# Performance work log

Measured on AMD Instinct MI355X. Metric: run time of the kernel, lower is better.

Reference implementation:

```python
import jax, jax.numpy as jnp
import numpy as np

B, S = 1, 2048
HIDDEN = 2560
NH, NKV, HD = 32, 8, 128
GS = 128  # awq group size
ROPE_THETA = 1000000.0


def dequant_q4(qweight, scales, qzeros):
    """Unpack int4 AWQ weights -> dense [K, N] float weight.
    qweight: [K//8, N] int32, 8 nibbles packed along the input (K) dim.
    scales/qzeros: [K//GS, N]. w = (nibble - zero) * scale.
    """
    K8, N = qweight.shape
    shifts = jnp.arange(8, dtype=jnp.int32) * 4
    nib = (qweight[:, None, :] >> shifts[None, :, None]) & 0xF  # [K//8, 8, N]
    w = nib.reshape(K8 * 8, N).astype(scales.dtype)             # [K, N]
    z = jnp.repeat(qzeros.astype(scales.dtype), GS, axis=0)     # [K, N]
    s = jnp.repeat(scales, GS, axis=0)                          # [K, N]
    return (w - z) * s


def linear_q4(x, qw, sc, qz, bias=None):
    w = dequant_q4(qw, sc, qz)                     # [K, N]
    y = jnp.einsum('bsk,kn->bsn', x, w)
    return y + bias if bias is not None else y


def rotate_half(x):
    x1, x2 = jnp.split(x, 2, axis=-1)
    return jnp.concatenate([-x2, x1], axis=-1)


def apply_rope(q, k, cos, sin):
    # cos/sin: [B, S, HD] -> broadcast over heads at dim 2
    c = cos[:, :, None, :]
    s = sin[:, :, None, :]
    return q * c + rotate_half(q) * s, k * c + rotate_half(k) * s


def setup_inputs() -> dict:
    key = jax.random.key(0)
    ks = jax.random.split(key, 12)

    x = jax.random.normal(ks[0], (B, S, HIDDEN), dtype=jnp.float32)

    # genuine rotary embedding tables
    inv_freq = 1.0 / (ROPE_THETA ** (np.arange(0, HD, 2, dtype=np.float32) / HD))
    t = np.arange(S, dtype=np.float32)
    freqs = np.outer(t, inv_freq)                      # [S, HD/2]
    emb = np.concatenate([freqs, freqs], axis=-1)      # [S, HD]
    cos = jnp.asarray(np.cos(emb)[None], dtype=jnp.float32)  # [1, S, HD]
    sin = jnp.asarray(np.sin(emb)[None], dtype=jnp.float32)

    def mk_proj(kq, ksc, kz, K, N, group=GS):
        qw = jax.random.randint(kq, (K // 8, N), 0, 2**31 - 1, dtype=jnp.int32)
        sc = jax.random.normal(ksc, (K // group, N), dtype=jnp.float32) * 0.01
        qz = jax.random.randint(kz, (K // group, N), 0, 16, dtype=jnp.int32)
        return qw, sc, qz

    q_qweight, q_scales, q_qzeros = mk_proj(ks[1], ks[2], ks[3], HIDDEN, NH * HD)
    k_qweight, k_scales, k_qzeros = mk_proj(ks[4], ks[5], ks[6], HIDDEN, NKV * HD)
    v_qweight, v_scales, v_qzeros = mk_proj(ks[7], ks[8], ks[9], HIDDEN, NKV * HD)
    o_qweight, o_scales, o_qzeros = mk_proj(ks[10], ks[11], jax.random.fold_in(key, 99), NH * HD, HIDDEN)

    kb = jax.random.split(jax.random.fold_in(key, 7), 3)
    q_bias = jax.random.normal(kb[0], (NH * HD,), dtype=jnp.float32) * 0.02
    k_bias = jax.random.normal(kb[1], (NKV * HD,), dtype=jnp.float32) * 0.02
    v_bias = jax.random.normal(kb[2], (NKV * HD,), dtype=jnp.float32) * 0.02

    return dict(x=x, cos=cos, sin=sin,
                q_scales=q_scales, q_bias=q_bias,
                k_scales=k_scales, k_bias=k_bias,
                v_scales=v_scales, v_bias=v_bias,
                o_scales=o_scales,
                q_qweight=q_qweight, q_qzeros=q_qzeros,
                k_qweight=k_qweight, k_qzeros=k_qzeros,
                v_qweight=v_qweight, v_qzeros=v_qzeros,
                o_qweight=o_qweight, o_qzeros=o_qzeros)


def reference(x, cos, sin,
              q_scales, q_bias, k_scales, k_bias, v_scales, v_bias, o_scales,
              q_qweight, q_qzeros, k_qweight, k_qzeros,
              v_qweight, v_qzeros, o_qweight, o_qzeros):
    b, s, _ = x.shape
    xq = linear_q4(x, q_qweight, q_scales, q_qzeros, q_bias).reshape(b, s, NH, HD)
    xk = linear_q4(x, k_qweight, k_scales, k_qzeros, k_bias).reshape(b, s, NKV, HD)
    xv = linear_q4(x, v_qweight, v_scales, v_qzeros, v_bias).reshape(b, s, NKV, HD)

    xq, xk = apply_rope(xq, xk, cos, sin)

    # GQA: repeat KV heads to match query heads (prefill, start_pos=0)
    rep = NH // NKV
    xk = jnp.repeat(xk, rep, axis=2)   # [b, s, NH, HD]
    xv = jnp.repeat(xv, rep, axis=2)

    scale = 1.0 / jnp.sqrt(jnp.asarray(HD, dtype=xq.dtype))
    scores = jnp.einsum('bqhd,bkhd->bhqk', xq, xk) * scale  # [b, NH, s, s]
    causal = jnp.tril(jnp.ones((s, s), dtype=bool))
    scores = jnp.where(causal[None, None], scores, jnp.finfo(scores.dtype).min)
    attn = jax.nn.softmax(scores, axis=-1)
    out = jnp.einsum('bhqk,bkhd->bqhd', attn, xv).reshape(b, s, NH * HD)

    return linear_q4(out, o_qweight, o_scales, o_qzeros)  # [b, s, HIDDEN]
```

## Files before the change

### kernel.cpp

```cpp
#include <hip/hip_runtime.h>
#include <hip/hip_bf16.h>
#include <cstdint>

#define S_LEN 2048
#define HIDDEN 2560
#define NH 32
#define NKV 8
#define HD 128
#define GS 128

typedef __attribute__((ext_vector_type(8))) _Float16 half8v;
typedef __attribute__((ext_vector_type(2))) _Float16 half2v;
typedef __attribute__((ext_vector_type(4))) float f32x4;
typedef unsigned int uint;
typedef unsigned short ushort;

__device__ inline ushort f2h(float f) {
    _Float16 h = (_Float16)f;
    return __builtin_bit_cast(ushort, h);
}
__device__ inline float h2f(ushort u) {
    return (float)__builtin_bit_cast(_Float16, u);
}
__device__ inline uint pk2(ushort a, ushort b) { return (uint)a | ((uint)b << 16); }

__device__ __attribute__((always_inline)) inline void gl_lds16(const void* g, void* l) {
    __builtin_amdgcn_global_load_lds(
        (const __attribute__((address_space(1))) unsigned int*)g,
        (__attribute__((address_space(3))) unsigned int*)l, 16, 0, 0);
}

#define WAIT_LGKM0  asm volatile("s_waitcnt lgkmcnt(0)" ::: "memory")
#define WAIT_VM(N)  asm volatile("s_waitcnt vmcnt(" #N ")" ::: "memory")
#define RAW_BARRIER { __builtin_amdgcn_s_barrier(); __builtin_amdgcn_sched_barrier(0); }

__global__ __launch_bounds__(256) void prep_kernel(
    const float* __restrict__ X, ushort* __restrict__ Xf,
    const int* __restrict__ q_qw, const float* __restrict__ q_sc, const int* __restrict__ q_qz,
    const int* __restrict__ k_qw, const float* __restrict__ k_sc, const int* __restrict__ k_qz,
    const int* __restrict__ v_qw, const float* __restrict__ v_sc, const int* __restrict__ v_qz,
    ushort* __restrict__ WT)
{
    __shared__ __align__(16) char Ts[16384];
    const int bid = blockIdx.x;
    const int t   = threadIdx.x;

    if (bid < 2560) {
        const size_t base = (size_t)bid * 2048 + (size_t)t * 8;
        float4 a = *(const float4*)&X[base];
        float4 b = *(const float4*)&X[base + 4];
        uint4 hw = {pk2(f2h(a.x), f2h(a.y)), pk2(f2h(a.z), f2h(a.w)),
                    pk2(f2h(b.x), f2h(b.y)), pk2(f2h(b.z), f2h(b.w))};
        *(uint4*)&Xf[base] = hw;
        return;
    }

    const int b2 = bid - 2560;
    const int bx = b2 % 96;
    const int kt = b2 / 96;

    int nloc0, wtbase, Nw;
    const int* QW; const float* SC; const int* QZ;
    if (bx < 64)      { Nw = NH * HD;  nloc0 = bx * 64;        wtbase = bx * 64;
                        QW = q_qw; SC = q_sc; QZ = q_qz; }
    else if (bx < 80) { Nw = NKV * HD; nloc0 = (bx - 64) * 64; wtbase = 4096 + nloc0;
                        QW = k_qw; SC = k_sc; QZ = k_qz; }
    else              { Nw = NKV * HD; nloc0 = (bx - 80) * 64; wtbase = 5120 + nloc0;
                        QW = v_qw; SC = v_sc; QZ = v_qz; }

    const int k80 = kt * 16;
    const int nn  = t & 63;
    const float scf = SC[(size_t)kt * Nw + nloc0 + nn];
    const float zf  = (float)QZ[(size_t)kt * Nw + nloc0 + nn];
    ushort sch = f2h(scf);
    float schf = h2f(sch);
    ushort msc = f2h(-128.0f * schf);
    ushort nzs = f2h(-(zf * schf));
    half2v S2 = {__builtin_bit_cast(_Float16, sch), __builtin_bit_cast(_Float16, sch)};
    half2v M2 = {__builtin_bit_cast(_Float16, msc), __builtin_bit_cast(_Float16, msc)};
    half2v Z2 = {__builtin_bit_cast(_Float16, nzs), __builtin_bit_cast(_Float16, nzs)};

#pragma unroll
    for (int i = 0; i < 4; ++i) {
        int kw = i * 4 + (t >> 6);
        uint q = (uint)QW[(size_t)(k80 + kw) * Nw + nloc0 + nn];
        uint xn = q & 0x0F0F0F0Fu;
        uint yn = (q >> 4) & 0x0F0F0F0Fu;
        uint W0 = __builtin_amdgcn_perm(yn, xn, 0x0C040C00u);
        uint W1 = __builtin_amdgcn_perm(yn, xn, 0x0C050C01u);
        uint W2 = __builtin_amdgcn_perm(yn, xn, 0x0C060C02u);
        uint W3 = __builtin_amdgcn_perm(yn, xn, 0x0C070C03u);
        uint e0 = (W0 << 3) | 0x58005800u;
        uint e1 = (W1 << 3) | 0x58005800u;
        uint e2 = (W2 << 3) | 0x58005800u;
        uint e3 = (W3 << 3) | 0x58005800u;
        half2v w0 = __builtin_bit_cast(half2v, e0) * S2 + M2; w0 = w0 + Z2;
        half2v w1 = __builtin_bit_cast(half2v, e1) * S2 + M2; w1 = w1 + Z2;
        half2v w2 = __builtin_bit_cast(half2v, e2) * S2 + M2; w2 = w2 + Z2;
        half2v w3 = __builtin_bit_cast(half2v, e3) * S2 + M2; w3 = w3 + Z2;
        uint4 dw = {__builtin_bit_cast(uint, w0), __builtin_bit_cast(uint, w1),
                    __builtin_bit_cast(uint, w2), __builtin_bit_cast(uint, w3)};
        *(uint4*)(Ts + nn * 256 + ((kw * 16) ^ ((nn & 7) << 4))) = dw;
    }
    __syncthreads();
    const int kc = t & 15;
#pragma unroll
    for (int i = 0; i < 4; ++i) {
        int nr = i * 16 + (t >> 4);
        uint4 v = *(const uint4*)(Ts + nr * 256 + ((kc * 16) ^ ((nr & 7) << 4)));
        *(uint4*)&WT[(size_t)(wtbase + nr) * HIDDEN + kt * 128 + kc * 8] = v;
    }
}

__global__ __launch_bounds__(256) void qkv12_kernel(
    const ushort* __restrict__ Xf, const ushort* __restrict__ WT,
    const float* __restrict__ q_b, const float* __restrict__ k_b,
    const float* __restrict__ v_b,
    const float* __restrict__ cosb, const float* __restrict__ sinb,
    ushort* __restrict__ Qf, ushort* __restrict__ Kf,
    ushort* __restrict__ VfT)
{
    __shared__ __align__(16) char LDSB[65536];
    ushort* A0 = (ushort*)(LDSB);
    ushort* A1 = (ushort*)(LDSB + 16384);
    ushort* B0 = (ushort*)(LDSB + 32768);
    ushort* B1 = (ushort*)(LDSB + 49152);

    const int t  = threadIdx.x;
    const int w  = t >> 6;
    const int l  = t & 63;
    const int lg = l >> 4;
    const int lr = l & 15;
    const int wr = w >> 1;
    const int wc = w & 1;
    const int K  = HIDDEN;

    const int bid  = blockIdx.x;
    const int xcd  = bid & 7;
    const int j    = bid >> 3;
    const int nblk = xcd * 6 + (j >> 4);
    const int m0   = (j & 15) * 128;
    const int wtrow = nblk * 128;

    int region, nbase;
    const float* BI;
    if (nblk < 32)      { region = 0; nbase = nblk * 128;        BI = q_b; }
    else if (nblk < 40) { region = 1; nbase = (nblk - 32) * 128; BI = k_b; }
    else                { region = 2; nbase = (nblk - 40) * 128; BI = v_b; }

    const int ldsAw = w * 1024;
    size_t aoff[4], boff[4];
#pragma unroll
    for (int i = 0; i < 4; ++i) {
        int slot = i * 256 + t;
        int rm = slot >> 3, rc = slot & 7;
        aoff[i] = (size_t)(m0 + rm) * K + (size_t)((rc ^ (rm & 7)) * 8);
        boff[i] = (size_t)(wtrow + rm) * K + (size_t)((rc ^ (rm & 7)) * 8);
    }

    int ncm[4];
#pragma unroll
    for (int nf = 0; nf < 4; ++nf)
        ncm[nf] = wc * 32 + (nf & 1) * 16 + lr + ((nf & 2) ? 64 : 0);

    const int xorA = (lr & 7) << 4;
    int aroff[4][2], broff[4][2];
#pragma unroll
    for (int mf = 0; mf < 4; ++mf)
#pragma unroll
        for (int ks = 0; ks < 2; ++ks)
            aroff[mf][ks] = (((wr * 64 + mf * 16 + lr) * 128) + lg * 16 + ks * 64) ^ xorA;
#pragma unroll
    for (int nf = 0; nf < 4; ++nf)
#pragma unroll
        for (int ks = 0; ks < 2; ++ks)
            broff[nf][ks] = ((ncm[nf] * 128) + lg * 16 + ks * 64) ^ xorA;

    f32x4 macc[4][4];
#pragma unroll
    for (int mf = 0; mf < 4; ++mf)
#pragma unroll
        for (int nf = 0; nf < 4; ++nf) macc[mf][nf] = f32x4{0.f, 0.f, 0.f, 0.f};

#define QKV_STAGE(AH, BH, k0) { \
    gl_lds16(Xf + (k0) + aoff[0], (char*)(AH) + ldsAw); \
    gl_lds16(Xf + (k0) + aoff[1], (char*)(AH) + 4096 + ldsAw); \
    gl_lds16(Xf + (k0) + aoff[2], (char*)(AH) + 8192 + ldsAw); \
    gl_lds16(Xf + (k0) + aoff[3], (char*)(AH) + 12288 + ldsAw); \
    gl_lds16(WT + (k0) + boff[0], (char*)(BH) + ldsAw); \
    gl_lds16(WT + (k0) + boff[1], (char*)(BH) + 4096 + ldsAw); \
    gl_lds16(WT + (k0) + boff[2], (char*)(BH) + 8192 + ldsAw); \
    gl_lds16(WT + (k0) + boff[3], (char*)(BH) + 12288 + ldsAw); }

#define QKV_COMPUTE(AH, BT) { \
    _Pragma("unroll") \
    for (int ks = 0; ks < 2; ++ks) { \
        half8v av[4], bv[4]; \
        _Pragma("unroll") \
        for (int mf = 0; mf < 4; ++mf) \
            av[mf] = *(const half8v*)((const char*)(AH) + aroff[mf][ks]); \
        _Pragma("unroll") \
        for (int nf = 0; nf < 4; ++nf) \
            bv[nf] = *(const half8v*)((const char*)(BT) + broff[nf][ks]); \
        _Pragma("unroll") \
        for (int mf = 0; mf < 4; ++mf) \
            _Pragma("unroll") \
            for (int nf = 0; nf < 4; ++nf) \
                macc[mf][nf] = __builtin_amdgcn_mfma_f32_16x16x32_f16(av[mf], bv[nf], macc[mf][nf], 0, 0, 0); \
    } }

    QKV_STAGE(A0, B0, 0);
    WAIT_VM(0);
    RAW_BARRIER;

    for (int g = 0; g < 19; ++g) {
        QKV_STAGE(A1, B1, (2 * g + 1) * 64);
        QKV_COMPUTE(A0, B0);
        WAIT_VM(0);
        RAW_BARRIER;
        QKV_STAGE(A0, B0, (2 * g + 2) * 64);
        QKV_COMPUTE(A1, B1);
        WAIT_VM(0);
        RAW_BARRIER;
    }
    QKV_STAGE(A1, B1, 39 * 64);
    QKV_COMPUTE(A0, B0);
    WAIT_VM(0);
    RAW_BARRIER;
    QKV_COMPUTE(A1, B1);

#pragma unroll
    for (int nf = 0; nf < 4; ++nf) {
        float bv = BI[nbase + ncm[nf]];
#pragma unroll
        for (int mf = 0; mf < 4; ++mf)
#pragma unroll
            for (int r = 0; r < 4; ++r) macc[mf][nf][r] += bv;
    }

    if (region == 2) {
        WAIT_LGKM0;
        RAW_BARRIER;
        ushort* EP = (ushort*)LDSB;
#pragma unroll
        for (int mf = 0; mf < 4; ++mf)
#pragma unroll
            for (int r = 0; r < 4; ++r) {
                int row = wr * 64 + mf * 16 + lg * 4 + r;
#pragma unroll
                for (int nf = 0; nf < 4; ++nf)
                    EP[row * 130 + ncm[nf]] = f2h(macc[mf][nf][r]);
            }
        WAIT_LGKM0;
        RAW_BARRIER;
        const int c   = t >> 1;
        const int seg = (t & 1) * 64;
        ushort* dst = &VfT[(size_t)(nbase + c) * S_LEN + m0 + seg];
#pragma unroll
        for (int g8 = 0; g8 < 8; ++g8) {
            ushort buf[8];
#pragma unroll
            for (int jj = 0; jj < 8; ++jj)
                buf[jj] = EP[(seg + g8 * 8 + jj) * 130 + c];
            *(uint4*)(dst + g8 * 8) = *(uint4*)buf;
        }
    } else {
        ushort* OF = (region == 0) ? Qf : Kf;
        const int No = (region == 0) ? NH * HD : NKV * HD;
        const float osc = (region == 0)
            ? 0.08838834764831845f * 1.44269504088896341f : 1.0f;
#pragma unroll
        for (int mf = 0; mf < 4; ++mf)
#pragma unroll
            for (int r = 0; r < 4; ++r) {
                int row = m0 + wr * 64 + mf * 16 + lg * 4 + r;
                const float* cb = &cosb[(size_t)row * HD];
                const float* sb = &sinb[(size_t)row * HD];
#pragma unroll
                for (int nf = 0; nf < 2; ++nf) {
                    int d = wc * 32 + nf * 16 + lr;
                    float a = macc[mf][nf][r];
                    float b = macc[mf][nf + 2][r];
                    float o1 = (a * cb[d]      - b * sb[d])      * osc;
                    float o2 = (b * cb[d + 64] + a * sb[d + 64]) * osc;
                    OF[(size_t)row * No + nbase + d]      = f2h(o1);
                    OF[(size_t)row * No + nbase + d + 64] = f2h(o2);
                }
            }
    }
#undef QKV_STAGE
#undef QKV_COMPUTE
}

__global__ __launch_bounds__(256) void oproj8_kernel(
    const ushort* __restrict__ Xb, const int* __restrict__ QW,
    const float* __restrict__ SC, const int* __restrict__ QZ,
    float* __restrict__ Y)
{
    __shared__ __align__(16) char LDSB[65536];
    ushort* A0 = (ushort*)(LDSB);
    ushort* A1 = (ushort*)(LDSB + 16384);
    ushort* B0 = (ushort*)(LDSB + 32768);
    ushort* B1 = (ushort*)(LDSB + 49152);

    const int t  = threadIdx.x;
    const int w  = t >> 6;
    const int l  = t & 63;
    const int lg = l >> 4;
    const int lr = l & 15;
    const int wr = w >> 1;
    const int wc = w & 1;
    const int K  = NH * HD;
    const int N  = HIDDEN;

    const int bid = blockIdx.x;
    const int swz = (bid & 7) * 40 + (bid >> 3);
    const int n0  = (swz % 20) * 128;
    const int m0  = (swz / 20) * 128;

    const int ldsAw = w * 1024;
    size_t aoff[4];
#pragma unroll
    for (int i = 0; i < 4; ++i) {
        int slot = i * 256 + t;
        int am = slot >> 3, ac = slot & 7;
        aoff[i] = (size_t)(m0 + am) * K + (size_t)((ac ^ (am & 7)) * 8);
    }
    const int bn  = t & 127;
    const int bk0 = (t >> 7) * 4;
    int bwoff[4];
#pragma unroll
    for (int j = 0; j < 4; ++j)
        bwoff[j] = (bn * 128 + (bk0 + j) * 16) ^ ((bn & 7) << 4);

    const int xorA = (lr & 7) << 4;
    int aroff[4][2], broff[4][2];
#pragma unroll
    for (int mf = 0; mf < 4; ++mf)
#pragma unroll
        for (int ks = 0; ks < 2; ++ks)
            aroff[mf][ks] = (((wr * 64 + mf * 16 + lr) * 128) + lg * 16 + ks * 64) ^ xorA;
#pragma unroll
    for (int nf = 0; nf < 4; ++nf)
#pragma unroll
        for (int ks = 0; ks < 2; ++ks)
            broff[nf][ks] = (((wc * 64 + nf * 16 + lr) * 128) + lg * 16 + ks * 64) ^ xorA;

    f32x4 macc[4][4];
#pragma unroll
    for (int mf = 0; mf < 4; ++mf)
#pragma unroll
        for (int nf = 0; nf < 4; ++nf) macc[mf][nf] = f32x4{0.f, 0.f, 0.f, 0.f};
    uint qr[4];
    float scf, zf;

#define OP_QW(tile) { int g8 = (tile) * 8; int gg = (tile) >> 1; \
    _Pragma("unroll") \
    for (int j = 0; j < 4; ++j) \
        qr[j] = (uint)QW[(size_t)(g8 + bk0 + j) * N + n0 + bn]; \
    scf = SC[(size_t)gg * N + n0 + bn]; \
    zf  = (float)QZ[(size_t)gg * N + n0 + bn]; }

#define OP_STAGE_A(AH, k0) { \
    gl_lds16(Xb + (k0) + aoff[0], (char*)(AH) + ldsAw); \
    gl_lds16(Xb + (k0) + aoff[1], (char*)(AH) + 4096 + ldsAw); \
    gl_lds16(Xb + (k0) + aoff[2], (char*)(AH) + 8192 + ldsAw); \
    gl_lds16(Xb + (k0) + aoff[3], (char*)(AH) + 12288 + ldsAw); }

#define OP_BWRITE(BT) { \
    ushort sch = f2h(scf); \
    float schf = h2f(sch); \
    ushort msc = f2h(-128.0f * schf); \
    ushort nzs = f2h(-(zf * schf)); \
    half2v S2 = {__builtin_bit_cast(_Float16, sch), __builtin_bit_cast(_Float16, sch)}; \
    half2v M2 = {__builtin_bit_cast(_Float16, msc), __builtin_bit_cast(_Float16, msc)}; \
    half2v Z2 = {__builtin_bit_cast(_Float16, nzs), __builtin_bit_cast(_Float16, nzs)}; \
    _Pragma("unroll") \
    for (int j = 0; j < 4; ++j) { \
        uint q = qr[j]; \
        uint xn = q & 0x0F0F0F0Fu; \
        uint yn = (q >> 4) & 0x0F0F0F0Fu; \
        uint4 dw; \
        uint W0 = __builtin_amdgcn_perm(yn, xn, 0x0C040C00u); \
        uint W1 = __builtin_amdgcn_perm(yn, xn, 0x0C050C01u); \
        uint W2 = __builtin_amdgcn_perm(yn, xn, 0x0C060C02u); \
        uint W3 = __builtin_amdgcn_perm(yn, xn, 0x0C070C03u); \
        uint e0 = (W0 << 3) | 0x58005800u; \
        uint e1 = (W1 << 3) | 0x58005800u; \
        uint e2 = (W2 << 3) | 0x58005800u; \
        uint e3 = (W3 << 3) | 0x58005800u; \
        half2v w0 = __builtin_bit_cast(half2v, e0) * S2 + M2; w0 = w0 + Z2; \
        half2v w1 = __builtin_bit_cast(half2v, e1) * S2 + M2; w1 = w1 + Z2; \
        half2v w2 = __builtin_bit_cast(half2v, e2) * S2 + M2; w2 = w2 + Z2; \
        half2v w3 = __builtin_bit_cast(half2v, e3) * S2 + M2; w3 = w3 + Z2; \
        dw.x = __builtin_bit_cast(uint, w0); \
        dw.y = __builtin_bit_cast(uint, w1); \
        dw.z = __builtin_bit_cast(uint, w2); \
        dw.w = __builtin_bit_cast(uint, w3); \
        *(uint4*)((char*)(BT) + bwoff[j]) = dw; \
    } }

#define OP_COMPUTE(AH, BT) { \
    _Pragma("unroll") \
    for (int ks = 0; ks < 2; ++ks) { \
        half8v av[4], bv[4]; \
        _Pragma("unroll") \
        for (int mf = 0; mf < 4; ++mf) \
            av[mf] = *(const half8v*)((const char*)(AH) + aroff[mf][ks]); \
        _Pragma("unroll") \
        for (int nf = 0; nf < 4; ++nf) \
            bv[nf] = *(const half8v*)((const char*)(BT) + broff[nf][ks]); \
        _Pragma("unroll") \
        for (int mf = 0; mf < 4; ++mf) \
            _Pragma("unroll") \
            for (int nf = 0; nf < 4; ++nf) \
                macc[mf][nf] = __builtin_amdgcn_mfma_f32_16x16x32_f16(av[mf], bv[nf], macc[mf][nf], 0, 0, 0); \
    } }

    OP_QW(0);
    OP_BWRITE(B0);
    OP_STAGE_A(A0, 0);
    OP_QW(1);
    WAIT_LGKM0;
    WAIT_VM(6);
    RAW_BARRIER;

    for (int g = 0; g < 31; ++g) {
        OP_STAGE_A(A1, (2 * g + 1) * 64);
        OP_COMPUTE(A0, B0);
        OP_BWRITE(B1);
        OP_QW(2 * g + 2);
        WAIT_LGKM0;
        WAIT_VM(6);
        RAW_BARRIER;
        OP_STAGE_A(A0, (2 * g + 2) * 64);
        OP_COMPUTE(A1, B1);
        OP_BWRITE(B0);
        OP_QW(2 * g + 3);
        WAIT_LGKM0;
        WAIT_VM(6);
        RAW_BARRIER;
    }
    OP_STAGE_A(A1, 63 * 64);
    OP_COMPUTE(A0, B0);
    OP_BWRITE(B1);
    WAIT_LGKM0;
    WAIT_VM(0);
    RAW_BARRIER;
    OP_COMPUTE(A1, B1);

#pragma unroll
    for (int mf = 0; mf < 4; ++mf)
#pragma unroll
        for (int r = 0; r < 4; ++r) {
            int row = m0 + wr * 64 + mf * 16 + lg * 4 + r;
#pragma unroll
            for (int nf = 0; nf < 4; ++nf)
                Y[(size_t)row * N + n0 + wc * 64 + nf * 16 + lr] = macc[mf][nf][r];
        }
#undef OP_QW
#undef OP_STAGE_A
#undef OP_BWRITE
#undef OP_COMPUTE
}

__global__ __launch_bounds__(256) void attn_mfma_kernel(
    const ushort* __restrict__ Qh,
    const ushort* __restrict__ Kh,
    const ushort* __restrict__ Vt,
    ushort* __restrict__ AO)
{
    __shared__ ushort Ks0[32 * 128];
    __shared__ ushort Ks1[32 * 128];
    __shared__ ushort Vs0[128 * 32];
    __shared__ ushort Vs1[128 * 32];
    __shared__ __align__(16) char PsB[4 * 1280];

    const int h  = blockIdx.x;
    const int qb = gridDim.y - 1 - blockIdx.y;
    const int s0 = qb * 64;
    const int t  = threadIdx.x;
    const int w  = t >> 6;
    const int l  = t & 63;
    const int lg = l >> 4;
    const int lr = l & 15;
    const int kvh = h >> 2;
    const int qw = s0 + w * 16;
    const int q  = qw + lr;

    half8v qf[4];
#pragma unroll
    for (int d = 0; d < 4; ++d) {
        size_t off = (size_t)q * (NH * HD) + h * HD + d * 32 + lg * 8;
        qf[d] = *(const half8v*)&Qh[off];
    }

    f32x4 o[8];
#pragma unroll
    for (int i = 0; i < 8; ++i) o[i] = f32x4{0.f, 0.f, 0.f, 0.f};
    float m = -1e30f, lsum = 0.f;
    char* pw = PsB + w * 1280;

#define ATTN_STAGE(KB, VB, k0) { \
    _Pragma("unroll") \
    for (int i = 0; i < 2; ++i) { \
        int slot = w * 128 + i * 64 + l; \
        int mr = slot >> 4, c = slot & 15; \
        size_t goff = (size_t)((k0) + mr) * (NKV * HD) + kvh * HD + ((c ^ (mr & 7)) * 8); \
        gl_lds16(Kh + goff, (char*)(KB) + (w * 128 + i * 64) * 16); \
    } \
    _Pragma("unroll") \
    for (int i = 0; i < 2; ++i) { \
        int slot = w * 128 + i * 64 + l; \
        int dim = slot >> 2, c = slot & 3; \
        size_t goff = (size_t)(kvh * HD + dim) * S_LEN + (k0) + ((c ^ ((dim >> 1) & 3)) * 8); \
        gl_lds16(Vt + goff, (char*)(VB) + (w * 128 + i * 64) * 16); \
    } }

#define ATTN_TILE(KSF, VSS, k0) \
    if ((k0) <= qw + 15) { \
        f32x4 s_[2]; \
        s_[0] = f32x4{0.f, 0.f, 0.f, 0.f}; \
        s_[1] = f32x4{0.f, 0.f, 0.f, 0.f}; \
        _Pragma("unroll") \
        for (int d = 0; d < 4; ++d) { \
            _Pragma("unroll") \
            for (int nt2 = 0; nt2 < 2; ++nt2) { \
                int row = nt2 * 16 + lr; \
                int off = row * 256 + ((d * 64 + lg * 16) ^ ((row & 7) << 4)); \
                half8v kf = *(const half8v*)((const char*)(KSF) + off); \
                s_[nt2] = __builtin_amdgcn_mfma_f32_16x16x32_f16(kf, qf[d], s_[nt2], 0, 0, 0); \
            } \
        } \
        float sv[8]; \
        _Pragma("unroll") \
        for (int nt2 = 0; nt2 < 2; ++nt2) \
            _Pragma("unroll") \
            for (int r = 0; r < 4; ++r) { \
                int kv = (k0) + nt2 * 16 + lg * 4 + r; \
                sv[nt2 * 4 + r] = (kv <= q) ? s_[nt2][r] : -1e30f; \
            } \
        float mx = sv[0]; \
        _Pragma("unroll") \
        for (int j = 1; j < 8; ++j) mx = fmaxf(mx, sv[j]); \
        mx = fmaxf(mx, __shfl_xor(mx, 16)); \
        mx = fmaxf(mx, __shfl_xor(mx, 32)); \
        float mnew = fmaxf(m, mx); \
        float resc = __builtin_amdgcn_exp2f(m - mnew); \
        m = mnew; \
        float p_[8], ps = 0.f; \
        _Pragma("unroll") \
        for (int j = 0; j < 8; ++j) { p_[j] = __builtin_amdgcn_exp2f(sv[j] - mnew); ps += p_[j]; } \
        ps += __shfl_xor(ps, 16); \
        ps += __shfl_xor(ps, 32); \
        lsum = lsum * resc + ps; \
        _Pragma("unroll") \
        for (int dt = 0; dt < 8; ++dt) \
            _Pragma("unroll") \
            for (int r = 0; r < 4; ++r) o[dt][r] *= resc; \
        uint2 w0_ = {pk2(f2h(p_[0]), f2h(p_[1])), pk2(f2h(p_[2]), f2h(p_[3]))}; \
        uint2 w1_ = {pk2(f2h(p_[4]), f2h(p_[5])), pk2(f2h(p_[6]), f2h(p_[7]))}; \
        *(uint2*)(pw + lr * 80 + lg * 8)      = w0_; \
        *(uint2*)(pw + lr * 80 + 32 + lg * 8) = w1_; \
        asm volatile("s_waitcnt lgkmcnt(0)" ::: "memory"); \
        half8v pf = *(const half8v*)(pw + lr * 80 + lg * 16); \
        _Pragma("unroll") \
        for (int dt = 0; dt < 8; ++dt) { \
            int dim = dt * 16 + lr; \
            half8v vf = *(const half8v*)((const char*)(VSS) + dim * 64 + ((lg * 16) ^ (((dim >> 1) & 3) << 4))); \
            o[dt] = __builtin_amdgcn_mfma_f32_16x16x32_f16(vf, pf, o[dt], 0, 0, 0); \
        } \
    }

    const int ntiles = qb * 2 + 2;

    ATTN_STAGE(Ks0, Vs0, 0);
    WAIT_VM(0);
    RAW_BARRIER;

    for (int kt = 0; kt < ntiles; kt += 2) {
        if (kt + 1 < ntiles) ATTN_STAGE(Ks1, Vs1, (kt + 1) * 32);
        ATTN_TILE(Ks0, Vs0, kt * 32);
        WAIT_VM(0);
        RAW_BARRIER;
        if (kt + 2 < ntiles) ATTN_STAGE(Ks0, Vs0, (kt + 2) * 32);
        ATTN_TILE(Ks1, Vs1, (kt + 1) * 32);
        WAIT_VM(0);
        RAW_BARRIER;
    }

    float inv = 1.f / lsum;
    ushort* dst = &AO[(size_t)q * (NH * HD) + h * HD];
#pragma unroll
    for (int dt = 0; dt < 8; ++dt) {
        uint2 ov = {pk2(f2h(o[dt][0] * inv), f2h(o[dt][1] * inv)),
                    pk2(f2h(o[dt][2] * inv), f2h(o[dt][3] * inv))};
        *(uint2*)(dst + dt * 16 + lg * 4) = ov;
    }
#undef ATTN_STAGE
#undef ATTN_TILE
}

extern "C" void kernel_launch(void* const* d_in, const int* in_sizes, int n_in,
                              void* d_out, int out_size, void* d_ws, size_t ws_size,
                              hipStream_t stream)
{
    const float* x    = (const float*)d_in[0];
    const float* cosb = (const float*)d_in[1];
    const float* sinb = (const float*)d_in[2];
    const float* q_sc = (const float*)d_in[3];
    const float* q_b  = (const float*)d_in[4];
    const float* k_sc = (const float*)d_in[5];
    const float* k_b  = (const float*)d_in[6];
    const float* v_sc = (const float*)d_in[7];
    const float* v_b  = (const float*)d_in[8];
    const float* o_sc = (const float*)d_in[9];
    const int* q_qw   = (const int*)d_in[10];
    const int* q_qz   = (const int*)d_in[11];
    const int* k_qw   = (const int*)d_in[12];
    const int* k_qz   = (const int*)d_in[13];
    const int* v_qw   = (const int*)d_in[14];
    const int* v_qz   = (const int*)d_in[15];
    const int* o_qw   = (const int*)d_in[16];
    const int* o_qz   = (const int*)d_in[17];
    float* out = (float*)d_out;

    char* ws = (char*)d_ws;
    ushort* Xf   = (ushort*)ws;
    ushort* AOf  = (ushort*)ws;
    ushort* WT   = (ushort*)(ws + (size_t)10 * 1024 * 1024);
    ushort* Qf   = (ushort*)(ws + (size_t)40 * 1024 * 1024);
    ushort* Kf   = (ushort*)(ws + (size_t)56 * 1024 * 1024);
    ushort* VfT  = (ushort*)(ws + (size_t)64 * 1024 * 1024);

    prep_kernel<<<4480, 256, 0, stream>>>(
        x, Xf,
        q_qw, q_sc, q_qz, k_qw, k_sc, k_qz, v_qw, v_sc, v_qz, WT);

    qkv12_kernel<<<768, 256, 0, stream>>>(
        Xf, WT, q_b, k_b, v_b, cosb, sinb, Qf, Kf, VfT);

    attn_mfma_kernel<<<dim3(NH, S_LEN / 64), 256, 0, stream>>>(Qf, Kf, VfT, AOf);

    oproj8_kernel<<<320, 256, 0, stream>>>(
        AOf, o_qw, o_sc, o_qz, out);
}
```

Baseline: 254.3 us.

## Pre-dequantize o_proj weights in a separate kernel and stream fp16 tiles

Adds a prep2 kernel that dequantizes the int4 o_proj weights into a transposed fp16 buffer, reusing a shared tile-dequant helper factored out of prep_kernel. The o_proj GEMM then loads both A and B tiles with direct global-to-LDS copies instead of unpacking nibbles inside the main loop. It also remaps blocks to XCD groups by column range. The aim is to remove the per-tile dequant ALU work and the LDS write stalls from the GEMM loop. In exchange it adds an extra launch and roughly 20 MB of fp16 weight writes and reads, and it waits on vmcnt(0) each stage, which reduces load overlap.

After: 238.3 us, median of 2. 1.07x faster.

```diff
diff --git a/kernel.cpp b/kernel.cpp
--- a/kernel.cpp
+++ b/kernel.cpp
@@ -34,40 +34,11 @@
 #define WAIT_VM(N)  asm volatile("s_waitcnt vmcnt(" #N ")" ::: "memory")
 #define RAW_BARRIER { __builtin_amdgcn_s_barrier(); __builtin_amdgcn_sched_barrier(0); }
 
-__global__ __launch_bounds__(256) void prep_kernel(
-    const float* __restrict__ X, ushort* __restrict__ Xf,
-    const int* __restrict__ q_qw, const float* __restrict__ q_sc, const int* __restrict__ q_qz,
-    const int* __restrict__ k_qw, const float* __restrict__ k_sc, const int* __restrict__ k_qz,
-    const int* __restrict__ v_qw, const float* __restrict__ v_sc, const int* __restrict__ v_qz,
-    ushort* __restrict__ WT)
+__device__ __attribute__((always_inline)) inline void wdq_tile(
+    const int* __restrict__ QW, const float* __restrict__ SC,
+    const int* __restrict__ QZ, ushort* __restrict__ Wout,
+    int Nw, int Kout, int nloc0, int wtbase, int kt, int t, char* Ts)
 {
-    __shared__ __align__(16) char Ts[16384];
-    const int bid = blockIdx.x;
-    const int t   = threadIdx.x;
-
-    if (bid < 2560) {
-        const size_t base = (size_t)bid * 2048 + (size_t)t * 8;
-        float4 a = *(const float4*)&X[base];
-        float4 b = *(const float4*)&X[base + 4];
-        uint4 hw = {pk2(f2h(a.x), f2h(a.y)), pk2(f2h(a.z), f2h(a.w)),
-                    pk2(f2h(b.x), f2h(b.y)), pk2(f2h(b.z), f2h(b.w))};
-        *(uint4*)&Xf[base] = hw;
-        return;
-    }
-
-    const int b2 = bid - 2560;
-    const int bx = b2 % 96;
-    const int kt = b2 / 96;
-
-    int nloc0, wtbase, Nw;
-    const int* QW; const float* SC; const int* QZ;
-    if (bx < 64)      { Nw = NH * HD;  nloc0 = bx * 64;        wtbase = bx * 64;
-                        QW = q_qw; SC = q_sc; QZ = q_qz; }
-    else if (bx < 80) { Nw = NKV * HD; nloc0 = (bx - 64) * 64; wtbase = 4096 + nloc0;
-                        QW = k_qw; SC = k_sc; QZ = k_qz; }
-    else              { Nw = NKV * HD; nloc0 = (bx - 80) * 64; wtbase = 5120 + nloc0;
-                        QW = v_qw; SC = v_sc; QZ = v_qz; }
-
     const int k80 = kt * 16;
     const int nn  = t & 63;
     const float scf = SC[(size_t)kt * Nw + nloc0 + nn];
@@ -108,8 +79,57 @@
     for (int i = 0; i < 4; ++i) {
         int nr = i * 16 + (t >> 4);
         uint4 v = *(const uint4*)(Ts + nr * 256 + ((kc * 16) ^ ((nr & 7) << 4)));
-        *(uint4*)&WT[(size_t)(wtbase + nr) * HIDDEN + kt * 128 + kc * 8] = v;
-    }
+        *(uint4*)&Wout[(size_t)(wtbase + nr) * Kout + kt * 128 + kc * 8] = v;
+    }
+}
+
+__global__ __launch_bounds__(256) void prep_kernel(
+    const float* __restrict__ X, ushort* __restrict__ Xf,
+    const int* __restrict__ q_qw, const float* __restrict__ q_sc, const int* __restrict__ q_qz,
+    const int* __restrict__ k_qw, const float* __restrict__ k_sc, const int* __restrict__ k_qz,
+    const int* __restrict__ v_qw, const float* __restrict__ v_sc, const int* __restrict__ v_qz,
+    ushort* __restrict__ WT)
+{
+    __shared__ __align__(16) char Ts[16384];
+    const int bid = blockIdx.x;
+    const int t   = threadIdx.x;
+
+    if (bid < 2560) {
+        const size_t base = (size_t)bid * 2048 + (size_t)t * 8;
+        float4 a = *(const float4*)&X[base];
+        float4 b = *(const float4*)&X[base + 4];
+        uint4 hw = {pk2(f2h(a.x), f2h(a.y)), pk2(f2h(a.z), f2h(a.w)),
+                    pk2(f2h(b.x), f2h(b.y)), pk2(f2h(b.z), f2h(b.w))};
+        *(uint4*)&Xf[base] = hw;
+        return;
+    }
+
+    const int b2 = bid - 2560;
+    const int bx = b2 % 96;
+    const int kt = b2 / 96;
+
+    int nloc0, wtbase, Nw;
+    const int* QW; const float* SC; const int* QZ;
+    if (bx < 64)      { Nw = NH * HD;  nloc0 = bx * 64;        wtbase = bx * 64;
+                        QW = q_qw; SC = q_sc; QZ = q_qz; }
+    else if (bx < 80) { Nw = NKV * HD; nloc0 = (bx - 64) * 64; wtbase = 4096 + nloc0;
+                        QW = k_qw; SC = k_sc; QZ = k_qz; }
+    else              { Nw = NKV * HD; nloc0 = (bx - 80) * 64; wtbase = 5120 + nloc0;
+                        QW = v_qw; SC = v_sc; QZ = v_qz; }
+
+    wdq_tile(QW, SC, QZ, WT, Nw, HIDDEN, nloc0, wtbase, kt, t, Ts);
+}
+
+__global__ __launch_bounds__(256) void prep2_kernel(
+    const int* __restrict__ o_qw, const float* __restrict__ o_sc,
+    const int* __restrict__ o_qz, ushort* __restrict__ WTO)
+{
+    __shared__ __align__(16) char Ts[16384];
+    const int bid = blockIdx.x;
+    const int t   = threadIdx.x;
+    const int bx  = bid % 40;
+    const int kt  = bid / 40;
+    wdq_tile(o_qw, o_sc, o_qz, WTO, HIDDEN, NH * HD, bx * 64, bx * 64, kt, t, Ts);
 }
 
 __global__ __launch_bounds__(256) void qkv12_kernel(
@@ -292,9 +312,8 @@
 #undef QKV_COMPUTE
 }
 
-__global__ __launch_bounds__(256) void oproj8_kernel(
-    const ushort* __restrict__ Xb, const int* __restrict__ QW,
-    const float* __restrict__ SC, const int* __restrict__ QZ,
+__global__ __launch_bounds__(256) void oproj9_kernel(
+    const ushort* __restrict__ Xb, const ushort* __restrict__ WTO,
     float* __restrict__ Y)
 {
     __shared__ __align__(16) char LDSB[65536];
@@ -313,25 +332,23 @@
     const int K  = NH * HD;
     const int N  = HIDDEN;
 
-    const int bid = blockIdx.x;
-    const int swz = (bid & 7) * 40 + (bid >> 3);
-    const int n0  = (swz % 20) * 128;
-    const int m0  = (swz / 20) * 128;
+    const int bid  = blockIdx.x;
+    const int xcd  = bid & 7;
+    const int grp  = xcd >> 1;
+    const int j    = (bid >> 3) * 2 + (xcd & 1);
+    const int nblk = grp * 5 + (j % 5);
+    const int m0   = (j / 5) * 128;
+    const int n0   = nblk * 128;
 
     const int ldsAw = w * 1024;
-    size_t aoff[4];
+    size_t aoff[4], boff[4];
 #pragma unroll
     for (int i = 0; i < 4; ++i) {
         int slot = i * 256 + t;
-        int am = slot >> 3, ac = slot & 7;
-        aoff[i] = (size_t)(m0 + am) * K + (size_t)((ac ^ (am & 7)) * 8);
-    }
-    const int bn  = t & 127;
-    const int bk0 = (t >> 7) * 4;
-    int bwoff[4];
-#pragma unroll
-    for (int j = 0; j < 4; ++j)
-        bwoff[j] = (bn * 128 + (bk0 + j) * 16) ^ ((bn & 7) << 4);
+        int rm = slot >> 3, rc = slot & 7;
+        aoff[i] = (size_t)(m0 + rm) * K + (size_t)((rc ^ (rm & 7)) * 8);
+        boff[i] = (size_t)(n0 + rm) * K + (size_t)((rc ^ (rm & 7)) * 8);
+    }
 
     const int xorA = (lr & 7) << 4;
     int aroff[4][2], broff[4][2];
@@ -351,54 +368,16 @@
     for (int mf = 0; mf < 4; ++mf)
 #pragma unroll
         for (int nf = 0; nf < 4; ++nf) macc[mf][nf] = f32x4{0.f, 0.f, 0.f, 0.f};
-    uint qr[4];
-    float scf, zf;
-
-#define OP_QW(tile) { int g8 = (tile) * 8; int gg = (tile) >> 1; \
-    _Pragma("unroll") \
-    for (int j = 0; j < 4; ++j) \
-        qr[j] = (uint)QW[(size_t)(g8 + bk0 + j) * N + n0 + bn]; \
-    scf = SC[(size_t)gg * N + n0 + bn]; \
-    zf  = (float)QZ[(size_t)gg * N + n0 + bn]; }
-
-#define OP_STAGE_A(AH, k0) { \
+
+#define OP_STAGE(AH, BH, k0) { \
     gl_lds16(Xb + (k0) + aoff[0], (char*)(AH) + ldsAw); \
     gl_lds16(Xb + (k0) + aoff[1], (char*)(AH) + 4096 + ldsAw); \
     gl_lds16(Xb + (k0) + aoff[2], (char*)(AH) + 8192 + ldsAw); \
-    gl_lds16(Xb + (k0) + aoff[3], (char*)(AH) + 12288 + ldsAw); }
-
-#define OP_BWRITE(BT) { \
-    ushort sch = f2h(scf); \
-    float schf = h2f(sch); \
-    ushort msc = f2h(-128.0f * schf); \
-    ushort nzs = f2h(-(zf * schf)); \
-    half2v S2 = {__builtin_bit_cast(_Float16, sch), __builtin_bit_cast(_Float16, sch)}; \
-    half2v M2 = {__builtin_bit_cast(_Float16, msc), __builtin_bit_cast(_Float16, msc)}; \
-    half2v Z2 = {__builtin_bit_cast(_Float16, nzs), __builtin_bit_cast(_Float16, nzs)}; \
-    _Pragma("unroll") \
-    for (int j = 0; j < 4; ++j) { \
-        uint q = qr[j]; \
-        uint xn = q & 0x0F0F0F0Fu; \
-        uint yn = (q >> 4) & 0x0F0F0F0Fu; \
-        uint4 dw; \
-        uint W0 = __builtin_amdgcn_perm(yn, xn, 0x0C040C00u); \
-        uint W1 = __builtin_amdgcn_perm(yn, xn, 0x0C050C01u); \
-        uint W2 = __builtin_amdgcn_perm(yn, xn, 0x0C060C02u); \
-        uint W3 = __builtin_amdgcn_perm(yn, xn, 0x0C070C03u); \
-        uint e0 = (W0 << 3) | 0x58005800u; \
-        uint e1 = (W1 << 3) | 0x58005800u; \
-        uint e2 = (W2 << 3) | 0x58005800u; \
-        uint e3 = (W3 << 3) | 0x58005800u; \
-        half2v w0 = __builtin_bit_cast(half2v, e0) * S2 + M2; w0 = w0 + Z2; \
-        half2v w1 = __builtin_bit_cast(half2v, e1) * S2 + M2; w1 = w1 + Z2; \
-        half2v w2 = __builtin_bit_cast(half2v, e2) * S2 + M2; w2 = w2 + Z2; \
-        half2v w3 = __builtin_bit_cast(half2v, e3) * S2 + M2; w3 = w3 + Z2; \
-        dw.x = __builtin_bit_cast(uint, w0); \
-        dw.y = __builtin_bit_cast(uint, w1); \
-        dw.z = __builtin_bit_cast(uint, w2); \
-        dw.w = __builtin_bit_cast(uint, w3); \
-        *(uint4*)((char*)(BT) + bwoff[j]) = dw; \
-    } }
+    gl_lds16(Xb + (k0) + aoff[3], (char*)(AH) + 12288 + ldsAw); \
+    gl_lds16(WTO + (k0) + boff[0], (char*)(BH) + ldsAw); \
+    gl_lds16(WTO + (k0) + boff[1], (char*)(BH) + 4096 + ldsAw); \
+    gl_lds16(WTO + (k0) + boff[2], (char*)(BH) + 8192 + ldsAw); \
+    gl_lds16(WTO + (k0) + boff[3], (char*)(BH) + 12288 + ldsAw); }
 
 #define OP_COMPUTE(AH, BT) { \
     _Pragma("unroll") \
@@ -417,34 +396,22 @@
                 macc[mf][nf] = __builtin_amdgcn_mfma_f32_16x16x32_f16(av[mf], bv[nf], macc[mf][nf], 0, 0, 0); \
     } }
 
-    OP_QW(0);
-    OP_BWRITE(B0);
-    OP_STAGE_A(A0, 0);
-    OP_QW(1);
-    WAIT_LGKM0;
-    WAIT_VM(6);
+    OP_STAGE(A0, B0, 0);
+    WAIT_VM(0);
     RAW_BARRIER;
 
     for (int g = 0; g < 31; ++g) {
-        OP_STAGE_A(A1, (2 * g + 1) * 64);
+        OP_STAGE(A1, B1, (2 * g + 1) * 64);
         OP_COMPUTE(A0, B0);
-        OP_BWRITE(B1);
-        OP_QW(2 * g + 2);
-        WAIT_LGKM0;
-        WAIT_VM(6);
-        RAW_BARRIER;
-        OP_STAGE_A(A0, (2 * g + 2) * 64);
+        WAIT_VM(0);
+        RAW_BARRIER;
+        OP_STAGE(A0, B0, (2 * g + 2) * 64);
         OP_COMPUTE(A1, B1);
-        OP_BWRITE(B0);
-        OP_QW(2 * g + 3);
-        WAIT_LGKM0;
-        WAIT_VM(6);
-        RAW_BARRIER;
-    }
-    OP_STAGE_A(A1, 63 * 64);
+        WAIT_VM(0);
+        RAW_BARRIER;
+    }
+    OP_STAGE(A1, B1, 63 * 64);
     OP_COMPUTE(A0, B0);
-    OP_BWRITE(B1);
-    WAIT_LGKM0;
     WAIT_VM(0);
     RAW_BARRIER;
     OP_COMPUTE(A1, B1);
@@ -458,9 +425,7 @@
             for (int nf = 0; nf < 4; ++nf)
                 Y[(size_t)row * N + n0 + wc * 64 + nf * 16 + lr] = macc[mf][nf][r];
         }
-#undef OP_QW
-#undef OP_STAGE_A
-#undef OP_BWRITE
+#undef OP_STAGE
 #undef OP_COMPUTE
 }
 
@@ -629,6 +594,7 @@
     ushort* Xf   = (ushort*)ws;
     ushort* AOf  = (ushort*)ws;
     ushort* WT   = (ushort*)(ws + (size_t)10 * 1024 * 1024);
+    ushort* WTO  = (ushort*)(ws + (size_t)16 * 1024 * 1024);
     ushort* Qf   = (ushort*)(ws + (size_t)40 * 1024 * 1024);
     ushort* Kf   = (ushort*)(ws + (size_t)56 * 1024 * 1024);
     ushort* VfT  = (ushort*)(ws + (size_t)64 * 1024 * 1024);
@@ -640,8 +606,9 @@
     qkv12_kernel<<<768, 256, 0, stream>>>(
         Xf, WT, q_b, k_b, v_b, cosb, sinb, Qf, Kf, VfT);
 
+    prep2_kernel<<<1280, 256, 0, stream>>>(o_qw, o_sc, o_qz, WTO);
+
     attn_mfma_kernel<<<dim3(NH, S_LEN / 64), 256, 0, stream>>>(Qf, Kf, VfT, AOf);
 
-    oproj8_kernel<<<320, 256, 0, stream>>>(
-        AOf, o_qw, o_sc, o_qz, out);
-}
+    oproj9_kernel<<<320, 256, 0, stream>>>(AOf, WTO, out);
+}
```
